# Optimization experiments

Hardware: AMD Instinct MI355X
Metric: run time of the kernel (lower is better)

Reference implementation:

```python
import jax, jax.numpy as jnp
import numpy as np

NUM_HEADS = 16


def setup_inputs() -> dict:
    key = jax.random.key(0)
    ks = jax.random.split(key, 5)
    B, N, C = 4, 2048, 1024
    x = jax.random.normal(ks[0], (B, N, C), dtype=jnp.float32)
    mask = jax.random.randint(ks[1], (B, N), 0, 2, dtype=jnp.int32)
    W_qkv = jax.random.normal(ks[2], (C, 3 * C), dtype=jnp.float32) * (C ** -0.5)
    W_proj = jax.random.normal(ks[3], (C, C), dtype=jnp.float32) * (C ** -0.5)
    b_proj = jnp.zeros((C,), dtype=jnp.float32)
    return {"x": x, "mask": mask, "W_qkv": W_qkv, "W_proj": W_proj, "b_proj": b_proj}


def reference(x, mask, W_qkv, W_proj, b_proj):
    B, N, C = x.shape
    H = NUM_HEADS
    hd = C // H
    scale = hd ** -0.5
    # qkv projection -> [3, B, H, N, hd]
    qkv = (x @ W_qkv).reshape(B, N, 3, H, hd).transpose(2, 0, 3, 1, 4)
    q, k, v = qkv[0], qkv[1], qkv[2]
    attn = jnp.einsum('bhqd,bhkd->bhqk', q, k) * scale  # [B,H,N,N]
    add_mask = (mask[:, None, None, :] != 1).astype(jnp.float32) * -10000.0
    attn = jax.nn.softmax(attn + add_mask, axis=-1)
    out = jnp.einsum('bhqk,bhkd->bhqd', attn, v)  # [B,H,N,hd]
    out = out.transpose(0, 2, 1, 3).reshape(B, N, C)
    return out @ W_proj + b_proj
```

## Files before the change

kernel.cpp:

```cpp
#include <hip/hip_runtime.h>

typedef unsigned short u16;
typedef unsigned int u32;
typedef unsigned long long u64;
typedef __attribute__((ext_vector_type(8))) short short8;
typedef __attribute__((ext_vector_type(4))) float f32x4;

#define QSCALE 0.18033688f

__device__ __forceinline__ u16 f2bf(float f) {
  u32 u = __builtin_bit_cast(u32, f);
  u += 0x7fffu + ((u >> 16) & 1u);
  return (u16)(u >> 16);
}

__device__ __forceinline__ float fexp2(float x) {
#if __has_builtin(__builtin_amdgcn_exp2f)
  return __builtin_amdgcn_exp2f(x);
#else
  return exp2f(x);
#endif
}

__device__ __forceinline__ void glds16(u16* lds, const u16* g) {
  __builtin_amdgcn_global_load_lds(
      (const __attribute__((address_space(1))) u32*)g,
      (__attribute__((address_space(3))) u32*)lds, 16, 0, 0);
}

#define MFMA(a, b, c) __builtin_amdgcn_mfma_f32_16x16x32_bf16((a), (b), (c), 0, 0, 0)


__global__ __launch_bounds__(256) void prep(const float* __restrict__ x,
                                            const int* __restrict__ mask,
                                            const float* __restrict__ Wqkv,
                                            const float* __restrict__ Wproj,
                                            u16* __restrict__ xb,
                                            u16* __restrict__ wqkvt,
                                            u16* __restrict__ wprojt,
                                            int* __restrict__ s2t,
                                            int* __restrict__ nkbuf) {
  __shared__ float tile[64][65];
  __shared__ int wtot[4];
  __shared__ int wbase[5];
  const int bid = blockIdx.x, t = threadIdx.x;

  if (bid < 8192) {
    int i = bid * 256 + t;
    float4 v = ((const float4*)x)[i];
    union { u16 s[4]; u64 ll; } u;
    u.s[0] = f2bf(v.x); u.s[1] = f2bf(v.y); u.s[2] = f2bf(v.z); u.s[3] = f2bf(v.w);
    ((u64*)xb)[i] = u.ll;
    return;
  }
  if (bid < 9216) {
    const float* Wm; u16* Wt; int Cc, bj, bi;
    if (bid < 8960) { int tt = bid - 8192; Wm = Wqkv;  Wt = wqkvt;  Cc = 3072; bj = tt % 48; bi = tt / 48; }
    else            { int tt = bid - 8960; Wm = Wproj; Wt = wprojt; Cc = 1024; bj = tt & 15; bi = tt >> 4; }
    const int r = t >> 4, c4 = (t & 15) << 2;
    for (int rr = r; rr < 64; rr += 16) {
      float4 v = *(const float4*)&Wm[(size_t)(bi * 64 + rr) * Cc + bj * 64 + c4];
      tile[rr][c4] = v.x; tile[rr][c4 + 1] = v.y; tile[rr][c4 + 2] = v.z; tile[rr][c4 + 3] = v.w;
    }
    __syncthreads();
    for (int rr = r; rr < 64; rr += 16) {
      union { u16 s[4]; u64 ll; } u;
      u.s[0] = f2bf(tile[c4][rr]);
      u.s[1] = f2bf(tile[c4 + 1][rr]);
      u.s[2] = f2bf(tile[c4 + 2][rr]);
      u.s[3] = f2bf(tile[c4 + 3][rr]);
      *(u64*)&Wt[(size_t)(bj * 64 + rr) * 1024 + bi * 64 + c4] = u.ll;
    }
    return;
  }
  const int b = bid - 9216;
  const int lane = t & 63, w = t >> 6;
  int m8[8], c = 0;
  #pragma unroll
  for (int j = 0; j < 8; j++) {
    m8[j] = (mask[b * 2048 + t * 8 + j] == 1);
    c += m8[j];
  }
  int incl = c;
  #pragma unroll
  for (int off = 1; off < 64; off <<= 1) {
    int v = __shfl_up(incl, off);
    if (lane >= off) incl += v;
  }
  if (lane == 63) wtot[w] = incl;
  __syncthreads();
  if (t == 0) {
    int s = 0;
    for (int i = 0; i < 4; i++) { wbase[i] = s; s += wtot[i]; }
    wbase[4] = s;
  }
  __syncthreads();
  const int nk = wbase[4];
  int urun = wbase[w] + incl - c;
  #pragma unroll
  for (int j = 0; j < 8; j++) {
    int tok = t * 8 + j;
    int slot = m8[j] ? urun : nk + (tok - urun);
    s2t[b * 2048 + slot] = b * 2048 + tok;
    urun += m8[j];
  }
  if (t == 0) nkbuf[b] = nk;
}

__global__ __launch_bounds__(256, 4) void gemm_fused(const u16* __restrict__ xb,
                                                     const u16* __restrict__ wqkvt,
                                                     const int* __restrict__ s2t,
                                                     const int* __restrict__ nkbuf,
                                                     u16* __restrict__ qbuf,
                                                     u16* __restrict__ kc,
                                                     u16* __restrict__ vtc) {
  __shared__ u16 Asm[128 * 64];
  __shared__ u16 Bsm[128 * 64];
  const int bid = blockIdx.x;
  const int role = bid >> 9;
  const int sub = bid & 511;
  const int tid = threadIdx.x, lane = tid & 63, w = tid >> 6;
  const int quad = lane >> 4, l15 = lane & 15;
  const int wm = (w >> 1) * 64, wn = (w & 1) * 64;
  const int srow = lane >> 3;
  const int gcc = ((lane & 7) ^ srow) * 8;
  const int rx8 = (l15 & 7);

  int m0, n0;
  if (role == 2) { m0 = (sub >> 6) * 128; n0 = (sub & 63) * 128; }
  else           { m0 = (sub & 63) * 128; n0 = (sub >> 6) * 128; }
  if (role == 1 && (m0 & 2047) >= nkbuf[m0 >> 11]) return;
  if (role == 2 && (n0 & 2047) >= nkbuf[n0 >> 11]) return;

  int arow[4], brow[4];
  #pragma unroll
  for (int c = 0; c < 4; ++c) {
    int rit = (w * 4 + c) * 8 + srow;
    if (role == 0)      { arow[c] = m0 + rit;            brow[c] = n0 + rit; }
    else if (role == 1) { arow[c] = s2t[m0 + rit];       brow[c] = 1024 + n0 + rit; }
    else                { arow[c] = 2048 + m0 + rit;     brow[c] = s2t[n0 + rit]; }
  }
  const u16 *Asrc = (role == 2) ? wqkvt : xb;
  const u16 *Bsrc = (role == 2) ? xb : wqkvt;

  f32x4 acc[4][4];
  #pragma unroll
  for (int i = 0; i < 4; i++)
    #pragma unroll
    for (int j = 0; j < 4; j++)
      #pragma unroll
      for (int r = 0; r < 4; r++) acc[i][j][r] = 0.f;

  for (int kt = 0; kt < 1024; kt += 64) {
    __syncthreads();
    #pragma unroll
    for (int c = 0; c < 4; ++c) {
      int chunk = w * 4 + c;
      glds16(&Asm[chunk * 512], &Asrc[(size_t)arow[c] * 1024 + kt + gcc]);
      glds16(&Bsm[chunk * 512], &Bsrc[(size_t)brow[c] * 1024 + kt + gcc]);
    }
    __syncthreads();
    #pragma unroll
    for (int ks = 0; ks < 2; ++ks) {
      int pc = ((ks * 4 + quad) ^ rx8) * 8;
      short8 av[4], bv[4];
      #pragma unroll
      for (int i = 0; i < 4; i++)
        av[i] = *(const short8*)&Asm[(wm + i * 16 + l15) * 64 + pc];
      #pragma unroll
      for (int j = 0; j < 4; j++)
        bv[j] = *(const short8*)&Bsm[(wn + j * 16 + l15) * 64 + pc];
      #pragma unroll
      for (int i = 0; i < 4; i++)
        #pragma unroll
        for (int j = 0; j < 4; j++)
          acc[i][j] = MFMA(av[i], bv[j], acc[i][j]);
    }
  }

  if (role == 2) {
    #pragma unroll
    for (int j = 0; j < 4; j++) {
      int col = n0 + wn + j * 16 + l15;
      int bb = col >> 11, sl = col & 2047;
      #pragma unroll
      for (int i = 0; i < 4; i++)
        #pragma unroll
        for (int r = 0; r < 4; r++) {
          int row = m0 + wm + i * 16 + quad * 4 + r;
          vtc[(size_t)(bb * 1024 + row) * 2048 + sl] = f2bf(acc[i][j][r]);
        }
    }
  } else {
    u16* dst = (role == 0) ? qbuf : kc;
    const float sc = (role == 0) ? QSCALE : 1.f;
    #pragma unroll
    for (int i = 0; i < 4; i++)
      #pragma unroll
      for (int j = 0; j < 4; j++) {
        int col = n0 + wn + j * 16 + l15;
        #pragma unroll
        for (int r = 0; r < 4; r++) {
          int row = m0 + wm + i * 16 + quad * 4 + r;
          dst[(size_t)row * 1024 + col] = f2bf(acc[i][j][r] * sc);
        }
      }
  }
}

__global__ __launch_bounds__(512, 4) void attn_kernel(const u16* __restrict__ q,
                                                      const u16* __restrict__ kc,
                                                      const u16* __restrict__ vtc,
                                                      const int* __restrict__ nkbuf,
                                                      u16* __restrict__ ao) {
  __shared__ u16 Ksm[2][2][64 * 64];
  __shared__ u16 Vsm[2][2][64 * 64];
  const int h = blockIdx.x, b = blockIdx.y, qt = blockIdx.z;
  const int tid = threadIdx.x, lane = tid & 63, w = tid >> 6;
  const int quad = lane >> 4, l15 = lane & 15;
  const int q0 = qt * 256 + w * 32;
  const int srow = lane >> 3;
  const int gcc = ((lane & 7) ^ srow) * 8;
  const int rx8 = (l15 & 7);
  const int nk = nkbuf[b];
  const int nt2 = (nk + 127) >> 7;
  const int quad8 = quad * 8;

  const int strow = w * 8 + srow;
  const int vrow = strow;
  const int prow = ((strow >> 4) & 1) * 32 + ((strow >> 2) & 3) * 8 +
                   ((strow >> 5) & 1) * 4 + (strow & 3);

  short8 ones;
  #pragma unroll
  for (int z = 0; z < 8; z++) ones[z] = (short)0x3F80;

  short8 qf[2][2];
  #pragma unroll
  for (int i = 0; i < 2; i++)
    #pragma unroll
    for (int ks = 0; ks < 2; ks++)
      qf[i][ks] = *(const short8*)&q[(size_t)(b * 2048 + q0 + i * 16 + l15) * 1024 +
                                     h * 64 + ks * 32 + quad * 8];

  f32x4 o[2][4], osum[2];
  #pragma unroll
  for (int i = 0; i < 2; i++) {
    #pragma unroll
    for (int r = 0; r < 4; r++) osum[i][r] = 0.f;
    #pragma unroll
    for (int jd = 0; jd < 4; jd++)
      #pragma unroll
      for (int r = 0; r < 4; r++) o[i][jd][r] = 0.f;
  }

#define STAGEKV(pb_, t_) {                                                             \
    const int k0s = (t_) * 128;                                                        \
    glds16(&Ksm[pb_][0][w * 512],                                                      \
           &kc[(size_t)(b * 2048 + k0s + prow) * 1024 + h * 64 + gcc]);                \
    glds16(&Vsm[pb_][0][w * 512],                                                      \
           &vtc[(size_t)(b * 1024 + h * 64 + vrow) * 2048 + k0s + gcc]);               \
    glds16(&Ksm[pb_][1][w * 512],                                                      \
           &kc[(size_t)(b * 2048 + k0s + 64 + prow) * 1024 + h * 64 + gcc]);           \
    glds16(&Vsm[pb_][1][w * 512],                                                      \
           &vtc[(size_t)(b * 1024 + h * 64 + vrow) * 2048 + k0s + 64 + gcc]);          \
  }

#define SUBTILE(pb_, st_, kbase_)                                                      \
  {                                                                                    \
    f32x4 s[4][2];                                                                     \
    _Pragma("unroll") for (int j = 0; j < 4; j++)                                      \
      _Pragma("unroll") for (int i = 0; i < 2; i++)                                    \
        _Pragma("unroll") for (int r = 0; r < 4; r++) s[j][i][r] = 0.f;                \
    _Pragma("unroll") for (int ks = 0; ks < 2; ks++) {                                 \
      int pc = ((ks * 4 + quad) ^ rx8) * 8;                                            \
      short8 kf[4];                                                                    \
      _Pragma("unroll") for (int j = 0; j < 4; j++)                                    \
        kf[j] = *(const short8*)&Ksm[pb_][st_][(j * 16 + l15) * 64 + pc];              \
      __builtin_amdgcn_s_setprio(1);                                                   \
      _Pragma("unroll") for (int j = 0; j < 4; j++)                                    \
        _Pragma("unroll") for (int i = 0; i < 2; i++)                                  \
          s[j][i] = MFMA(kf[j], qf[i][ks], s[j][i]);                                   \
      __builtin_amdgcn_s_setprio(0);                                                   \
    }                                                                                  \
    const bool tail = ((kbase_) + 64 > nk);                                            \
    short8 pf[2][2];                                                                   \
    _Pragma("unroll") for (int i = 0; i < 2; i++) {                                    \
      float p[4][4];                                                                   \
      if (!tail) {                                                                     \
        _Pragma("unroll") for (int j = 0; j < 4; j++)                                  \
          _Pragma("unroll") for (int r = 0; r < 4; r++)                                \
            p[j][r] = fexp2(s[j][i][r]);                                               \
      } else {                                                                         \
        _Pragma("unroll") for (int j = 0; j < 4; j++)                                  \
          _Pragma("unroll") for (int r = 0; r < 4; r++) {                              \
            int slot = (kbase_) + (j & 1) * 32 + quad8 + (j >> 1) * 4 + r;             \
            float e = fexp2(s[j][i][r]);                                               \
            p[j][r] = (slot < nk) ? e : 0.f;                                           \
          }                                                                            \
      }                                                                                \
      _Pragma("unroll") for (int ks = 0; ks < 2; ks++) {                               \
        union { u32 u[4]; short8 v; } pk;                                              \
        u32 a0 = __builtin_bit_cast(u32, p[ks][0]) + 0x8000u;                          \
        u32 a1 = __builtin_bit_cast(u32, p[ks][1]) + 0x8000u;                          \
        u32 a2 = __builtin_bit_cast(u32, p[ks][2]) + 0x8000u;                          \
        u32 a3 = __builtin_bit_cast(u32, p[ks][3]) + 0x8000u;                          \
        u32 b0 = __builtin_bit_cast(u32, p[ks + 2][0]) + 0x8000u;                      \
        u32 b1 = __builtin_bit_cast(u32, p[ks + 2][1]) + 0x8000u;                      \
        u32 b2 = __builtin_bit_cast(u32, p[ks + 2][2]) + 0x8000u;                      \
        u32 b3 = __builtin_bit_cast(u32, p[ks + 2][3]) + 0x8000u;                      \
        pk.u[0] = __builtin_amdgcn_perm(a1, a0, 0x07060302u);                          \
        pk.u[1] = __builtin_amdgcn_perm(a3, a2, 0x07060302u);                          \
        pk.u[2] = __builtin_amdgcn_perm(b1, b0, 0x07060302u);                          \
        pk.u[3] = __builtin_amdgcn_perm(b3, b2, 0x07060302u);                          \
        pf[i][ks] = pk.v;                                                              \
      }                                                                                \
    }                                                                                  \
    _Pragma("unroll") for (int ks = 0; ks < 2; ks++) {                                 \
      int pcv = ((ks * 4 + quad) ^ rx8) * 8;                                           \
      short8 vf[4];                                                                    \
      _Pragma("unroll") for (int jd = 0; jd < 4; jd++)                                 \
        vf[jd] = *(const short8*)&Vsm[pb_][st_][(jd * 16 + l15) * 64 + pcv];           \
      __builtin_amdgcn_s_setprio(1);                                                   \
      _Pragma("unroll") for (int i = 0; i < 2; i++) {                                  \
        osum[i] = MFMA(pf[i][ks], ones, osum[i]);                                      \
        _Pragma("unroll") for (int jd = 0; jd < 4; jd++)                               \
          o[i][jd] = MFMA(pf[i][ks], vf[jd], o[i][jd]);                                \
      }                                                                                \
      __builtin_amdgcn_s_setprio(0);                                                   \
    }                                                                                  \
  }

  STAGEKV(0, 0)
  __syncthreads();
  for (int t = 0; t < nt2; ++t) {
    const int k0 = t * 128;
    const int pb = t & 1;
    if (t + 1 < nt2) STAGEKV(pb ^ 1, t + 1)
    SUBTILE(pb, 0, k0)
    if (k0 + 64 < nk) SUBTILE(pb, 1, k0 + 64)
    __syncthreads();
  }
#undef SUBTILE
#undef STAGEKV

  #pragma unroll
  for (int i = 0; i < 2; i++)
    #pragma unroll
    for (int r = 0; r < 4; r++) {
      float inv = 1.f / osum[i][r];
      size_t row = (size_t)(b * 2048 + q0 + i * 16 + quad * 4 + r);
      #pragma unroll
      for (int jd = 0; jd < 4; jd++)
        ao[row * 1024 + h * 64 + jd * 16 + l15] = f2bf(o[i][jd][r] * inv);
    }
}

__global__ __launch_bounds__(256, 3) void gemm_proj(const u16* __restrict__ A,
                                                    const u16* __restrict__ Bt,
                                                    const float* __restrict__ bias,
                                                    float* __restrict__ out) {
  __shared__ u16 Asm[2][128 * 64];
  __shared__ u16 Bsm[2][128 * 64];
  const int tid = threadIdx.x, lane = tid & 63, w = tid >> 6;
  const int quad = lane >> 4, l15 = lane & 15;
  const int m0 = (blockIdx.x & 63) * 128, n0 = (blockIdx.x >> 6) * 128;
  const int wm = (w >> 1) * 64, wn = (w & 1) * 64;
  const int srow = lane >> 3;
  const int gcc = ((lane & 7) ^ srow) * 8;
  const int rx8 = (l15 & 7);
  f32x4 acc[4][4];
  #pragma unroll
  for (int i = 0; i < 4; i++)
    #pragma unroll
    for (int j = 0; j < 4; j++)
      #pragma unroll
      for (int r = 0; r < 4; r++) acc[i][j][r] = 0.f;

#define STAGEP(pb_, kt_) {                                                             \
    _Pragma("unroll") for (int c = 0; c < 4; ++c) {                                    \
      int chunk = w * 4 + c;                                                           \
      int row = chunk * 8 + srow;                                                      \
      glds16(&Asm[pb_][chunk * 512], &A[(size_t)(m0 + row) * 1024 + (kt_) + gcc]);     \
      glds16(&Bsm[pb_][chunk * 512], &Bt[(size_t)(n0 + row) * 1024 + (kt_) + gcc]);    \
    }                                                                                  \
  }

  STAGEP(0, 0)
  __syncthreads();
  for (int kt = 0, t = 0; kt < 1024; kt += 64, ++t) {
    const int pb = t & 1;
    if (kt + 64 < 1024) STAGEP(pb ^ 1, kt + 64)
    #pragma unroll
    for (int ks = 0; ks < 2; ++ks) {
      int pc = ((ks * 4 + quad) ^ rx8) * 8;
      short8 av[4], bv[4];
      #pragma unroll
      for (int i = 0; i < 4; i++)
        av[i] = *(const short8*)&Asm[pb][(wm + i * 16 + l15) * 64 + pc];
      #pragma unroll
      for (int j = 0; j < 4; j++)
        bv[j] = *(const short8*)&Bsm[pb][(wn + j * 16 + l15) * 64 + pc];
      #pragma unroll
      for (int i = 0; i < 4; i++)
        #pragma unroll
        for (int j = 0; j < 4; j++)
          acc[i][j] = MFMA(av[i], bv[j], acc[i][j]);
    }
    __syncthreads();
  }
#undef STAGEP

  #pragma unroll
  for (int j = 0; j < 4; j++) {
    int col = n0 + wn + j * 16 + l15;
    float bj = bias[col];
    #pragma unroll
    for (int i = 0; i < 4; i++) {
      #pragma unroll
      for (int r = 0; r < 4; r++) {
        int row = m0 + wm + i * 16 + quad * 4 + r;
        out[(size_t)row * 1024 + col] = acc[i][j][r] + bj;
      }
    }
  }
}

extern "C" void kernel_launch(void* const* d_in, const int* in_sizes, int n_in,
                              void* d_out, int out_size, void* d_ws, size_t ws_size,
                              hipStream_t stream) {
  (void)in_sizes; (void)n_in; (void)out_size; (void)ws_size;
  const float* x     = (const float*)d_in[0];
  const int*   mask  = (const int*)d_in[1];
  const float* Wqkv  = (const float*)d_in[2];
  const float* Wproj = (const float*)d_in[3];
  const float* bproj = (const float*)d_in[4];
  float* out = (float*)d_out;
  char* ws = (char*)d_ws;

  size_t off = 0;
  u16* xb     = (u16*)(ws + off); off += 8192ull * 1024 * 2;
  u16* wqkvt  = (u16*)(ws + off); off += 3072ull * 1024 * 2;
  u16* wprojt = (u16*)(ws + off); off += 1024ull * 1024 * 2;
  u16* qbuf   = (u16*)(ws + off); off += 8192ull * 1024 * 2;
  u16* kcbuf  = (u16*)(ws + off); off += 4096ull * 2048 * 2;
  u16* vtcbuf = (u16*)(ws + off); off += 4096ull * 2048 * 2;
  int* s2t    = (int*)(ws + off); off += 8192ull * 4;
  int* nkbuf  = (int*)(ws + off); off += 4 * 4;
  u16* aobuf  = xb;

  prep<<<9220, 256, 0, stream>>>(x, mask, Wqkv, Wproj, xb, wqkvt, wprojt, s2t, nkbuf);
  gemm_fused<<<1536, 256, 0, stream>>>(xb, wqkvt, s2t, nkbuf, qbuf, kcbuf, vtcbuf);
  attn_kernel<<<dim3(16, 4, 8), 512, 0, stream>>>(qbuf, kcbuf, vtcbuf, nkbuf, aobuf);
  gemm_proj<<<512, 256, 0, stream>>>(aobuf, wprojt, bproj, out);
}
```

Measured before the change: 212.2 us.

## Coarsen x conversion per thread and shrink proj GEMM tile to 128x64 single-buffered

The prep kernel's x-to-bf16 conversion now handles four float4s per thread, which cuts that part of the grid from 8192 blocks to 2048. The projection GEMM moves from a 128x128 double-buffered tile to a 128x64 single-buffered tile, doubling its grid to 1024 blocks and raising the occupancy hint to 4. The aim is less launch and scheduling overhead in prep and better CU fill in the projection GEMM. The cost is that the GEMM no longer overlaps global loads with MFMA and reuses less data per tile.

```diff
diff --git a/kernel.cpp b/kernel.cpp
--- a/kernel.cpp
+++ b/kernel.cpp
@@ -45,18 +45,28 @@
   __shared__ int wbase[5];
   const int bid = blockIdx.x, t = threadIdx.x;
 
-  if (bid < 8192) {
-    int i = bid * 256 + t;
-    float4 v = ((const float4*)x)[i];
+  if (bid < 2048) {
+    const int base = bid * 1024 + t;
+    float4 v0 = ((const float4*)x)[base];
+    float4 v1 = ((const float4*)x)[base + 256];
+    float4 v2 = ((const float4*)x)[base + 512];
+    float4 v3 = ((const float4*)x)[base + 768];
     union { u16 s[4]; u64 ll; } u;
-    u.s[0] = f2bf(v.x); u.s[1] = f2bf(v.y); u.s[2] = f2bf(v.z); u.s[3] = f2bf(v.w);
-    ((u64*)xb)[i] = u.ll;
+    u.s[0] = f2bf(v0.x); u.s[1] = f2bf(v0.y); u.s[2] = f2bf(v0.z); u.s[3] = f2bf(v0.w);
+    ((u64*)xb)[base] = u.ll;
+    u.s[0] = f2bf(v1.x); u.s[1] = f2bf(v1.y); u.s[2] = f2bf(v1.z); u.s[3] = f2bf(v1.w);
+    ((u64*)xb)[base + 256] = u.ll;
+    u.s[0] = f2bf(v2.x); u.s[1] = f2bf(v2.y); u.s[2] = f2bf(v2.z); u.s[3] = f2bf(v2.w);
+    ((u64*)xb)[base + 512] = u.ll;
+    u.s[0] = f2bf(v3.x); u.s[1] = f2bf(v3.y); u.s[2] = f2bf(v3.z); u.s[3] = f2bf(v3.w);
+    ((u64*)xb)[base + 768] = u.ll;
     return;
   }
-  if (bid < 9216) {
+  if (bid < 3072) {
     const float* Wm; u16* Wt; int Cc, bj, bi;
-    if (bid < 8960) { int tt = bid - 8192; Wm = Wqkv;  Wt = wqkvt;  Cc = 3072; bj = tt % 48; bi = tt / 48; }
-    else            { int tt = bid - 8960; Wm = Wproj; Wt = wprojt; Cc = 1024; bj = tt & 15; bi = tt >> 4; }
+    int tt = bid - 2048;
+    if (tt < 768) { Wm = Wqkv;  Wt = wqkvt;  Cc = 3072; bj = tt % 48; bi = tt / 48; }
+    else          { int t2 = tt - 768; Wm = Wproj; Wt = wprojt; Cc = 1024; bj = t2 & 15; bi = t2 >> 4; }
     const int r = t >> 4, c4 = (t & 15) << 2;
     for (int rr = r; rr < 64; rr += 16) {
       float4 v = *(const float4*)&Wm[(size_t)(bi * 64 + rr) * Cc + bj * 64 + c4];
@@ -73,7 +83,7 @@
     }
     return;
   }
-  const int b = bid - 9216;
+  const int b = bid - 3072;
   const int lane = t & 63, w = t >> 6;
   int m8[8], c = 0;
   #pragma unroll
@@ -356,63 +366,60 @@
     }
 }
 
-__global__ __launch_bounds__(256, 3) void gemm_proj(const u16* __restrict__ A,
+__global__ __launch_bounds__(256, 4) void gemm_proj(const u16* __restrict__ A,
                                                     const u16* __restrict__ Bt,
                                                     const float* __restrict__ bias,
                                                     float* __restrict__ out) {
-  __shared__ u16 Asm[2][128 * 64];
-  __shared__ u16 Bsm[2][128 * 64];
+  __shared__ u16 Asm[128 * 64];
+  __shared__ u16 Bsm[64 * 64];
   const int tid = threadIdx.x, lane = tid & 63, w = tid >> 6;
   const int quad = lane >> 4, l15 = lane & 15;
-  const int m0 = (blockIdx.x & 63) * 128, n0 = (blockIdx.x >> 6) * 128;
-  const int wm = (w >> 1) * 64, wn = (w & 1) * 64;
+  const int m0 = (blockIdx.x & 63) * 128, n0 = (blockIdx.x >> 6) * 64;
+  const int wm = (w >> 1) * 64, wn = (w & 1) * 32;
   const int srow = lane >> 3;
   const int gcc = ((lane & 7) ^ srow) * 8;
   const int rx8 = (l15 & 7);
-  f32x4 acc[4][4];
+  f32x4 acc[4][2];
   #pragma unroll
   for (int i = 0; i < 4; i++)
     #pragma unroll
-    for (int j = 0; j < 4; j++)
+    for (int j = 0; j < 2; j++)
       #pragma unroll
       for (int r = 0; r < 4; r++) acc[i][j][r] = 0.f;
 
-#define STAGEP(pb_, kt_) {                                                             \
-    _Pragma("unroll") for (int c = 0; c < 4; ++c) {                                    \
-      int chunk = w * 4 + c;                                                           \
-      int row = chunk * 8 + srow;                                                      \
-      glds16(&Asm[pb_][chunk * 512], &A[(size_t)(m0 + row) * 1024 + (kt_) + gcc]);     \
-      glds16(&Bsm[pb_][chunk * 512], &Bt[(size_t)(n0 + row) * 1024 + (kt_) + gcc]);    \
-    }                                                                                  \
-  }
-
-  STAGEP(0, 0)
-  __syncthreads();
-  for (int kt = 0, t = 0; kt < 1024; kt += 64, ++t) {
-    const int pb = t & 1;
-    if (kt + 64 < 1024) STAGEP(pb ^ 1, kt + 64)
+  for (int kt = 0; kt < 1024; kt += 64) {
+    __syncthreads();
+    #pragma unroll
+    for (int c = 0; c < 4; ++c) {
+      int chunk = w * 4 + c;
+      glds16(&Asm[chunk * 512], &A[(size_t)(m0 + chunk * 8 + srow) * 1024 + kt + gcc]);
+    }
+    #pragma unroll
+    for (int c = 0; c < 2; ++c) {
+      int chunk = w * 2 + c;
+      glds16(&Bsm[chunk * 512], &Bt[(size_t)(n0 + chunk * 8 + srow) * 1024 + kt + gcc]);
+    }
+    __syncthreads();
     #pragma unroll
     for (int ks = 0; ks < 2; ++ks) {
       int pc = ((ks * 4 + quad) ^ rx8) * 8;
-      short8 av[4], bv[4];
+      short8 av[4], bv[2];
       #pragma unroll
       for (int i = 0; i < 4; i++)
-        av[i] = *(const short8*)&Asm[pb][(wm + i * 16 + l15) * 64 + pc];
-      #pragma unroll
-      for (int j = 0; j < 4; j++)
-        bv[j] = *(const short8*)&Bsm[pb][(wn + j * 16 + l15) * 64 + pc];
+        av[i] = *(const short8*)&Asm[(wm + i * 16 + l15) * 64 + pc];
+      #pragma unroll
+      for (int j = 0; j < 2; j++)
+        bv[j] = *(const short8*)&Bsm[(wn + j * 16 + l15) * 64 + pc];
       #pragma unroll
       for (int i = 0; i < 4; i++)
         #pragma unroll
-        for (int j = 0; j < 4; j++)
+        for (int j = 0; j < 2; j++)
           acc[i][j] = MFMA(av[i], bv[j], acc[i][j]);
     }
-    __syncthreads();
-  }
-#undef STAGEP
-
-  #pragma unroll
-  for (int j = 0; j < 4; j++) {
+  }
+
+  #pragma unroll
+  for (int j = 0; j < 2; j++) {
     int col = n0 + wn + j * 16 + l15;
     float bj = bias[col];
     #pragma unroll
@@ -449,8 +456,8 @@
   int* nkbuf  = (int*)(ws + off); off += 4 * 4;
   u16* aobuf  = xb;
 
-  prep<<<9220, 256, 0, stream>>>(x, mask, Wqkv, Wproj, xb, wqkvt, wprojt, s2t, nkbuf);
+  prep<<<3076, 256, 0, stream>>>(x, mask, Wqkv, Wproj, xb, wqkvt, wprojt, s2t, nkbuf);
   gemm_fused<<<1536, 256, 0, stream>>>(xb, wqkvt, s2t, nkbuf, qbuf, kcbuf, vtcbuf);
   attn_kernel<<<dim3(16, 4, 8), 512, 0, stream>>>(qbuf, kcbuf, vtcbuf, nkbuf, aobuf);
-  gemm_proj<<<512, 256, 0, stream>>>(aobuf, wprojt, bproj, out);
-}
+  gemm_proj<<<1024, 256, 0, stream>>>(aobuf, wprojt, bproj, out);
+}
```

Result: no change. 212.6 us (+0.2%).
